# Kernel optimization log

Measured on AMD Instinct MI355X. Metric: run time of the kernel, lower is better.

Reference implementation:

```python
import jax, jax.numpy as jnp
import numpy as np

B, N, E = 16, 2048, 32768   # graphs per batch, nodes per graph, edges per graph
V, D, R, L = 50000, 256, 8, 2  # vocab, embed dim, num relations, gnn layers


def setup_inputs() -> dict:
    key = jax.random.key(0)
    ks = jax.random.split(key, 7)
    nodes = jax.random.randint(ks[0], (B, N), 0, V)
    edges = jax.random.randint(ks[1], (B, 2, E), 0, N)
    types = jax.random.randint(ks[2], (B, E), 0, R)
    emb = jax.random.normal(ks[3], (V, D), jnp.float32) * 0.02
    W = jax.random.normal(ks[4], (L, R, D, D), jnp.float32) * (1.0 / np.sqrt(D))
    W_root = jax.random.normal(ks[5], (L, D, D), jnp.float32) * (1.0 / np.sqrt(D))
    b = jnp.zeros((L, D), jnp.float32)
    return dict(nodes=nodes, edges=edges, types=types, emb=emb, W=W, W_root=W_root, b=b)


def _rgcn_layer(x, src, dst, etype, W, W_root, b):
    # x: [N,D]; src/dst/etype: [E]; W: [R,D,D]; W_root: [D,D]; b: [D]
    n = x.shape[0]
    xw = jnp.einsum('nd,rde->rne', x, W)          # per-relation transform [R,N,D]
    msgs = xw[etype, src]                          # gather per-edge messages [E,D]
    agg = jax.ops.segment_sum(msgs, dst, num_segments=n)          # scatter-add [N,D]
    deg = jax.ops.segment_sum(jnp.ones((src.shape[0],), x.dtype), dst, num_segments=n)
    return agg / jnp.maximum(deg, 1.0)[:, None] + x @ W_root + b  # mean aggr + self loop


def reference(nodes, edges, types, emb, W, W_root, b):
    x = emb[nodes]                                  # [B,N,D] per-sample embedding lookup
    src, dst = edges[:, 0], edges[:, 1]
    layer = jax.vmap(_rgcn_layer, in_axes=(0, 0, 0, 0, None, None, None))
    for l in range(L):
        x = layer(x, src, dst, types, W[l], W_root[l], b[l])
        if l < L - 1:
            x = jax.nn.relu(x)  # dropout is identity at inference
    return x
```

## Files before the change

kernel.cpp:

```cpp
#include <hip/hip_runtime.h>

#define BB 16
#define NN 2048
#define EE 32768
#define DD 256
#define RR 8
#define LL 2
#define BUCKETS (RR * NN)
#define TM 64

typedef unsigned short u16;
typedef __attribute__((__ext_vector_type__(8))) __bf16 bfx8;
typedef __attribute__((__ext_vector_type__(16))) float fx16;

__device__ __forceinline__ float blo(unsigned u){ union{unsigned x;float f;}c; c.x=u<<16; return c.f; }
__device__ __forceinline__ float bhi(unsigned u){ union{unsigned x;float f;}c; c.x=u&0xffff0000u; return c.f; }
__device__ __forceinline__ u16 f2bf(float f){ union{float f;unsigned u;}x; x.f=f;
    return (u16)((x.u + 0x7FFFu + ((x.u>>16)&1u))>>16); }
__device__ __forceinline__ unsigned pk2(float a, float b){
    return (unsigned)f2bf(a) | ((unsigned)f2bf(b)<<16); }

__global__ __launch_bounds__(256) void gather_k(const int* __restrict__ nodes,
                                                const float* __restrict__ emb,
                                                u16* __restrict__ x0,
                                                int b0, int bc)
{
    int t = blockIdx.x * 256 + threadIdx.x;
    int lane = t & 63;
    int row = t >> 6;
    if (row >= bc * NN) return;
    int bb = row / NN;
    int n  = row - bb * NN;
    int v  = nodes[(size_t)(b0 + bb) * NN + n];
    float4 val = *((const float4*)(emb + (size_t)v * DD) + lane);
    ushort4 o;
    o.x = f2bf(val.x); o.y = f2bf(val.y); o.z = f2bf(val.z); o.w = f2bf(val.w);
    *((ushort4*)(x0 + (size_t)row * DD) + lane) = o;
}

__global__ __launch_bounds__(256) void wt_k(const float* __restrict__ W,
                                            const float* __restrict__ Wroot,
                                            u16* __restrict__ Wf)
{
    __shared__ float tl[32][257];
    int ls = blockIdx.y;
    int l = ls / 9, seg = ls - l * 9;
    int kt = blockIdx.x;
    const float* src = (seg < 8) ? W + (size_t)(l * RR + seg) * DD * DD
                                 : Wroot + (size_t)l * DD * DD;
    int t = threadIdx.x;
    for (int k8 = 0; k8 < 32; ++k8)
        tl[k8][t] = src[(size_t)(kt * 32 + k8) * DD + t];
    __syncthreads();
    #pragma unroll
    for (int i = 0; i < 4; ++i) {
        int o = i * 256 + t;
        int fl = o & 63, ks2 = (o >> 6) & 1, nt8 = o >> 7;
        int n = nt8 * 32 + (fl & 31);
        int kb = ks2 * 16 + (fl >> 5) * 8;
        unsigned d0 = pk2(tl[kb + 0][n], tl[kb + 1][n]);
        unsigned d1 = pk2(tl[kb + 2][n], tl[kb + 3][n]);
        unsigned d2 = pk2(tl[kb + 4][n], tl[kb + 5][n]);
        unsigned d3 = pk2(tl[kb + 6][n], tl[kb + 7][n]);
        *(uint4*)(Wf + (((size_t)ls * 8 + kt) * 1024 + o) * 8) =
            make_uint4(d0, d1, d2, d3);
    }
}

__global__ __launch_bounds__(256) void count_k(const int* __restrict__ edges,
                                               const int* __restrict__ types,
                                               int* __restrict__ counts,
                                               int b0, int bc)
{
    int t = blockIdx.x * 256 + threadIdx.x;
    if (t >= bc * EE) return;
    int bb = t / EE;
    int e  = t - bb * EE;
    const int* eb = edges + (size_t)(b0 + bb) * 2 * EE;
    int dst = eb[EE + e];
    int r   = types[(size_t)(b0 + bb) * EE + e];
    atomicAdd(&counts[((size_t)bb * RR + r) * NN + dst], 1);
}

__global__ __launch_bounds__(256) void sect_k(const int* __restrict__ counts,
                                              int* __restrict__ secsum)
{
    __shared__ int red[256];
    int sec = blockIdx.x;
    int t = threadIdx.x;
    size_t base = (size_t)sec * NN;
    int s = 0;
    #pragma unroll
    for (int i = 0; i < 8; ++i) s += counts[base + t * 8 + i];
    red[t] = s;
    __syncthreads();
    for (int off = 128; off > 0; off >>= 1) {
        if (t < off) red[t] += red[t + off];
        __syncthreads();
    }
    if (t == 0) secsum[sec] = red[0];
}

__global__ __launch_bounds__(128) void base_k(const int* __restrict__ secsum,
                                              int* __restrict__ secbase, int nsec)
{
    int t = threadIdx.x;
    if (t >= nsec) return;
    int bb = t >> 3;
    int s = 0;
    for (int i = bb * 8; i < t; ++i) s += secsum[i];
    secbase[t] = s;
}

__global__ __launch_bounds__(256) void offs_k(const int* __restrict__ counts,
                                              const int* __restrict__ secbase,
                                              int* __restrict__ offsets,
                                              int* __restrict__ cursor)
{
    __shared__ int sums[256];
    int sec = blockIdx.x;
    int t = threadIdx.x;
    size_t base = (size_t)sec * NN;
    int v[8], s = 0;
    #pragma unroll
    for (int i = 0; i < 8; ++i) { v[i] = counts[base + t * 8 + i]; s += v[i]; }
    sums[t] = s;
    __syncthreads();
    for (int off = 1; off < 256; off <<= 1) {
        int x = (t >= off) ? sums[t - off] : 0;
        __syncthreads();
        sums[t] += x;
        __syncthreads();
    }
    int run = secbase[sec] + sums[t] - s;
    #pragma unroll
    for (int i = 0; i < 8; ++i) {
        offsets[base + t * 8 + i] = run;
        cursor[base + t * 8 + i]  = run;
        run += v[i];
    }
}

__global__ __launch_bounds__(256) void deg_from_counts(const int* __restrict__ counts,
                                                       float* __restrict__ deg,
                                                       int bc)
{
    int t = blockIdx.x * 256 + threadIdx.x;
    if (t >= bc * NN) return;
    int bb = t / NN;
    int n  = t - bb * NN;
    int d = 0;
    #pragma unroll
    for (int r = 0; r < RR; ++r)
        d += counts[((size_t)bb * RR + r) * NN + n];
    deg[t] = (float)d;
}

__global__ __launch_bounds__(256) void permute_k(const int* __restrict__ edges,
                                                 const int* __restrict__ types,
                                                 int* __restrict__ cursor,
                                                 int* __restrict__ edgeSrc,
                                                 int b0, int bc)
{
    int t = blockIdx.x * 256 + threadIdx.x;
    if (t >= bc * EE) return;
    int bb = t / EE;
    int e  = t - bb * EE;
    const int* eb = edges + (size_t)(b0 + bb) * 2 * EE;
    int src = eb[e];
    int dst = eb[EE + e];
    int r   = types[(size_t)(b0 + bb) * EE + e];
    int pos = atomicAdd(&cursor[((size_t)bb * RR + r) * NN + dst], 1);
    edgeSrc[(size_t)bb * EE + pos] = src;
}

template <int WRITE_BF16>
__global__ __launch_bounds__(512, 4) void rgcn_fused(
    const int* __restrict__ offsets, const int* __restrict__ counts,
    const int* __restrict__ edgeSrc, const u16* __restrict__ xin,
    const u16* __restrict__ Wf,
    const float* __restrict__ bias, const float* __restrict__ deg,
    float* __restrict__ outF, u16* __restrict__ outH, int relu)
{
    __shared__ __align__(16) u16 Af[2 * 16 * 64 * 8];
    __shared__ float sInv[TM];

    int t = threadIdx.x;
    int fl = t & 63;
    int wid = t >> 6;
    int bb = blockIdx.y;
    int m0 = blockIdx.x * TM;

    if (t < TM) sInv[t] = 1.0f / fmaxf(deg[(size_t)bb * NN + m0 + t], 1.0f);

    const u16* xb = xin + (size_t)bb * NN * DD;
    const int* es = edgeSrc + (size_t)bb * EE;

    int gid = t >> 4;
    int j16 = t & 15;
    int ks0 = j16 >> 1;
    int lh2 = j16 & 1;

    fx16 acc[2];
    #pragma unroll
    for (int mt = 0; mt < 2; ++mt)
        #pragma unroll
        for (int e = 0; e < 16; ++e) acc[mt][e] = 0.0f;

    int lh = fl >> 5;

    for (int seg = 0; seg < 9; ++seg) {
        __syncthreads();
        #pragma unroll
        for (int rr = 0; rr < 2; ++rr) {
            int row = gid * 2 + rr;
            int mt = row >> 5, m31 = row & 31;
            int flw = m31 + 32 * lh2;
            unsigned w0, w1, w2, w3, w4, w5, w6, w7;
            if (seg < 8) {
                float a[16];
                #pragma unroll
                for (int e = 0; e < 16; ++e) a[e] = 0.0f;
                int g = ((bb * RR + seg) * NN) + m0 + row;
                int start = offsets[g];
                int cnt   = counts[g];
                for (int jj = 0; jj < cnt; ++jj) {
                    int src = es[start + jj];
                    const u16* xr = xb + (size_t)src * DD;
                    uint4 p0 = *(const uint4*)(xr + j16 * 8);
                    uint4 p1 = *(const uint4*)(xr + 128 + j16 * 8);
                    a[0] += blo(p0.x); a[1] += bhi(p0.x);
                    a[2] += blo(p0.y); a[3] += bhi(p0.y);
                    a[4] += blo(p0.z); a[5] += bhi(p0.z);
                    a[6] += blo(p0.w); a[7] += bhi(p0.w);
                    a[8]  += blo(p1.x); a[9]  += bhi(p1.x);
                    a[10] += blo(p1.y); a[11] += bhi(p1.y);
                    a[12] += blo(p1.z); a[13] += bhi(p1.z);
                    a[14] += blo(p1.w); a[15] += bhi(p1.w);
                }
                w0 = pk2(a[0], a[1]);   w1 = pk2(a[2], a[3]);
                w2 = pk2(a[4], a[5]);   w3 = pk2(a[6], a[7]);
                w4 = pk2(a[8], a[9]);   w5 = pk2(a[10], a[11]);
                w6 = pk2(a[12], a[13]); w7 = pk2(a[14], a[15]);
            } else {
                const u16* xr = xb + (size_t)(m0 + row) * DD;
                uint4 p0 = *(const uint4*)(xr + j16 * 8);
                uint4 p1 = *(const uint4*)(xr + 128 + j16 * 8);
                w0 = p0.x; w1 = p0.y; w2 = p0.z; w3 = p0.w;
                w4 = p1.x; w5 = p1.y; w6 = p1.z; w7 = p1.w;
            }
            int c0 = ((mt * 16 + ks0) * 64 + ((flw + ks0) & 63)) * 8;
            int c1 = ((mt * 16 + ks0 + 8) * 64 + ((flw + ks0 + 8) & 63)) * 8;
            *(uint4*)&Af[c0] = make_uint4(w0, w1, w2, w3);
            *(uint4*)&Af[c1] = make_uint4(w4, w5, w6, w7);
        }
        __syncthreads();

        if (seg == 8) {
            #pragma unroll
            for (int mt = 0; mt < 2; ++mt)
                #pragma unroll
                for (int r = 0; r < 16; ++r) {
                    int rl = mt * 32 + (r & 3) + 8 * (r >> 2) + 4 * lh;
                    acc[mt][r] *= sInv[rl];
                }
        }

        const u16* Wseg = Wf + (size_t)seg * 65536;
        #pragma unroll 2
        for (int kt = 0; kt < 8; ++kt) {
            bfx8 bfr[2], af[2][2];
            #pragma unroll
            for (int ks2 = 0; ks2 < 2; ++ks2) {
                int ksA = kt * 2 + ks2;
                bfr[ks2] = *(const bfx8*)(Wseg + (size_t)kt * 8192 + wid * 1024
                                          + ks2 * 512 + fl * 8);
                af[0][ks2] = *(const bfx8*)&Af[((0  + ksA) * 64 + ((fl + ksA) & 63)) * 8];
                af[1][ks2] = *(const bfx8*)&Af[((16 + ksA) * 64 + ((fl + ksA) & 63)) * 8];
            }
            #pragma unroll
            for (int ks2 = 0; ks2 < 2; ++ks2) {
                acc[0] = __builtin_amdgcn_mfma_f32_32x32x16_bf16(af[0][ks2], bfr[ks2], acc[0], 0, 0, 0);
                acc[1] = __builtin_amdgcn_mfma_f32_32x32x16_bf16(af[1][ks2], bfr[ks2], acc[1], 0, 0, 0);
            }
        }
    }

    int col = wid * 32 + (fl & 31);
    float bv = bias[col];
    #pragma unroll
    for (int mt = 0; mt < 2; ++mt)
        #pragma unroll
        for (int r = 0; r < 16; ++r) {
            int row = m0 + mt * 32 + (r & 3) + 8 * (r >> 2) + 4 * lh;
            float v = acc[mt][r] + bv;
            if (relu) v = fmaxf(v, 0.0f);
            if (WRITE_BF16)
                outH[((size_t)bb * NN + row) * DD + col] = f2bf(v);
            else
                outF[((size_t)bb * NN + row) * DD + col] = v;
        }
}

extern "C" void kernel_launch(void* const* d_in, const int* in_sizes, int n_in,
                              void* d_out, int out_size, void* d_ws, size_t ws_size,
                              hipStream_t stream)
{
    const int*   nodes = (const int*)d_in[0];
    const int*   edges = (const int*)d_in[1];
    const int*   types = (const int*)d_in[2];
    const float* emb   = (const float*)d_in[3];
    const float* W     = (const float*)d_in[4];
    const float* Wroot = (const float*)d_in[5];
    const float* bias  = (const float*)d_in[6];
    float* out = (float*)d_out;

    const size_t wfElems = (size_t)LL * 9 * 8 * 1024 * 8;
    const size_t fixedBytes = wfElems * sizeof(u16) + 256 * sizeof(int);
    const size_t perBatchBytes =
        2 * (size_t)NN * DD * sizeof(u16) + (size_t)NN * sizeof(float) +
        (3 * (size_t)BUCKETS + EE) * sizeof(int);
    int BC = (int)((ws_size - fixedBytes) / perBatchBytes);
    if (BC > BB) BC = BB;
    if (BC < 1) BC = 1;

    u16* Wf      = (u16*)d_ws;
    int* secsum  = (int*)(Wf + wfElems);
    int* secbase = secsum + 128;
    u16* x0      = (u16*)(secbase + 128);
    u16* x1      = x0 + (size_t)BC * NN * DD;
    float* deg   = (float*)(x1 + (size_t)BC * NN * DD);
    int* counts  = (int*)(deg + (size_t)BC * NN);
    int* offsets = counts + (size_t)BC * BUCKETS;
    int* cursor  = offsets + (size_t)BC * BUCKETS;
    int* edgeSrc = cursor + (size_t)BC * BUCKETS;

    wt_k<<<dim3(8, LL * 9), 256, 0, stream>>>(W, Wroot, Wf);

    for (int b0 = 0; b0 < BB; b0 += BC) {
        int bc = BB - b0 < BC ? BB - b0 : BC;

        hipMemsetAsync(counts, 0, (size_t)bc * BUCKETS * sizeof(int), stream);
        gather_k<<<bc * 512, 256, 0, stream>>>(nodes, emb, x0, b0, bc);
        count_k<<<bc * (EE / 256), 256, 0, stream>>>(edges, types, counts, b0, bc);
        sect_k<<<bc * 8, 256, 0, stream>>>(counts, secsum);
        base_k<<<1, 128, 0, stream>>>(secsum, secbase, bc * 8);
        offs_k<<<bc * 8, 256, 0, stream>>>(counts, secbase, offsets, cursor);
        deg_from_counts<<<bc * (NN / 256), 256, 0, stream>>>(counts, deg, bc);
        permute_k<<<bc * (EE / 256), 256, 0, stream>>>(edges, types, cursor, edgeSrc, b0, bc);

        for (int l = 0; l < LL; ++l) {
            const u16* xin = (l == 0) ? x0 : x1;
            const u16* Wfl = Wf + (size_t)l * 9 * 65536;
            dim3 grid(NN / TM, bc);
            if (l == 0)
                rgcn_fused<1><<<grid, 512, 0, stream>>>(offsets, counts, edgeSrc,
                    xin, Wfl, bias + (size_t)l * DD, deg, nullptr, x1, 1);
            else
                rgcn_fused<0><<<grid, 512, 0, stream>>>(offsets, counts, edgeSrc,
                    xin, Wfl, bias + (size_t)l * DD, deg,
                    out + (size_t)b0 * NN * DD, nullptr, 0);
        }
    }
}
```

Baseline: 364.9 us.

## Merge prep kernels, double-buffer gathered A tiles, remap blocks across batches

Merges the preprocessing launches: weight transform with counts zeroing, embedding gather with edge counting, and a single per-batch scan that also computes inverse degree. This cuts launch count and removes the two-level section scan. In the fused layer kernel, the neighbour gather for the next relation segment now goes into a second LDS buffer while the MFMAs for the current segment run. The gather loop is unrolled by two, offsets and counts are staged in shared memory, and block indices are swizzled so neighbouring blocks work on different graphs. The cost is doubled LDS use, which may lower occupancy, and a single-block-per-batch scan that is very serial; the weight transform also now runs once per batch chunk.

```diff
diff --git a/kernel.cpp b/kernel.cpp
--- a/kernel.cpp
+++ b/kernel.cpp
@@ -19,141 +19,116 @@
     return (u16)((x.u + 0x7FFFu + ((x.u>>16)&1u))>>16); }
 __device__ __forceinline__ unsigned pk2(float a, float b){
     return (unsigned)f2bf(a) | ((unsigned)f2bf(b)<<16); }
-
-__global__ __launch_bounds__(256) void gather_k(const int* __restrict__ nodes,
-                                                const float* __restrict__ emb,
-                                                u16* __restrict__ x0,
-                                                int b0, int bc)
-{
-    int t = blockIdx.x * 256 + threadIdx.x;
-    int lane = t & 63;
-    int row = t >> 6;
-    if (row >= bc * NN) return;
-    int bb = row / NN;
-    int n  = row - bb * NN;
-    int v  = nodes[(size_t)(b0 + bb) * NN + n];
-    float4 val = *((const float4*)(emb + (size_t)v * DD) + lane);
-    ushort4 o;
-    o.x = f2bf(val.x); o.y = f2bf(val.y); o.z = f2bf(val.z); o.w = f2bf(val.w);
-    *((ushort4*)(x0 + (size_t)row * DD) + lane) = o;
-}
-
-__global__ __launch_bounds__(256) void wt_k(const float* __restrict__ W,
-                                            const float* __restrict__ Wroot,
-                                            u16* __restrict__ Wf)
-{
-    __shared__ float tl[32][257];
-    int ls = blockIdx.y;
-    int l = ls / 9, seg = ls - l * 9;
-    int kt = blockIdx.x;
-    const float* src = (seg < 8) ? W + (size_t)(l * RR + seg) * DD * DD
-                                 : Wroot + (size_t)l * DD * DD;
+__device__ __forceinline__ void acc8(float* a, uint4 p0, uint4 p1) {
+    a[0]+=blo(p0.x); a[1]+=bhi(p0.x); a[2]+=blo(p0.y); a[3]+=bhi(p0.y);
+    a[4]+=blo(p0.z); a[5]+=bhi(p0.z); a[6]+=blo(p0.w); a[7]+=bhi(p0.w);
+    a[8]+=blo(p1.x); a[9]+=bhi(p1.x); a[10]+=blo(p1.y); a[11]+=bhi(p1.y);
+    a[12]+=blo(p1.z); a[13]+=bhi(p1.z); a[14]+=blo(p1.w); a[15]+=bhi(p1.w);
+}
+
+__global__ __launch_bounds__(256) void prep0(const float* __restrict__ W,
+                                             const float* __restrict__ Wroot,
+                                             u16* __restrict__ Wf,
+                                             int* __restrict__ counts, int bc)
+{
     int t = threadIdx.x;
-    for (int k8 = 0; k8 < 32; ++k8)
-        tl[k8][t] = src[(size_t)(kt * 32 + k8) * DD + t];
-    __syncthreads();
-    #pragma unroll
-    for (int i = 0; i < 4; ++i) {
-        int o = i * 256 + t;
-        int fl = o & 63, ks2 = (o >> 6) & 1, nt8 = o >> 7;
-        int n = nt8 * 32 + (fl & 31);
-        int kb = ks2 * 16 + (fl >> 5) * 8;
-        unsigned d0 = pk2(tl[kb + 0][n], tl[kb + 1][n]);
-        unsigned d1 = pk2(tl[kb + 2][n], tl[kb + 3][n]);
-        unsigned d2 = pk2(tl[kb + 4][n], tl[kb + 5][n]);
-        unsigned d3 = pk2(tl[kb + 6][n], tl[kb + 7][n]);
-        *(uint4*)(Wf + (((size_t)ls * 8 + kt) * 1024 + o) * 8) =
-            make_uint4(d0, d1, d2, d3);
-    }
-}
-
-__global__ __launch_bounds__(256) void count_k(const int* __restrict__ edges,
-                                               const int* __restrict__ types,
-                                               int* __restrict__ counts,
-                                               int b0, int bc)
-{
-    int t = blockIdx.x * 256 + threadIdx.x;
-    if (t >= bc * EE) return;
-    int bb = t / EE;
-    int e  = t - bb * EE;
-    const int* eb = edges + (size_t)(b0 + bb) * 2 * EE;
-    int dst = eb[EE + e];
-    int r   = types[(size_t)(b0 + bb) * EE + e];
-    atomicAdd(&counts[((size_t)bb * RR + r) * NN + dst], 1);
-}
-
-__global__ __launch_bounds__(256) void sect_k(const int* __restrict__ counts,
-                                              int* __restrict__ secsum)
-{
-    __shared__ int red[256];
-    int sec = blockIdx.x;
-    int t = threadIdx.x;
-    size_t base = (size_t)sec * NN;
-    int s = 0;
-    #pragma unroll
-    for (int i = 0; i < 8; ++i) s += counts[base + t * 8 + i];
-    red[t] = s;
-    __syncthreads();
-    for (int off = 128; off > 0; off >>= 1) {
-        if (t < off) red[t] += red[t + off];
+    if (blockIdx.x < 8 * LL * 9) {
+        __shared__ float tl[32][257];
+        int kt = blockIdx.x & 7, ls = blockIdx.x >> 3;
+        int l = ls / 9, seg = ls - l * 9;
+        const float* src = (seg < 8) ? W + (size_t)(l * RR + seg) * DD * DD
+                                     : Wroot + (size_t)l * DD * DD;
+        for (int k8 = 0; k8 < 32; ++k8)
+            tl[k8][t] = src[(size_t)(kt * 32 + k8) * DD + t];
         __syncthreads();
-    }
-    if (t == 0) secsum[sec] = red[0];
-}
-
-__global__ __launch_bounds__(128) void base_k(const int* __restrict__ secsum,
-                                              int* __restrict__ secbase, int nsec)
-{
-    int t = threadIdx.x;
-    if (t >= nsec) return;
-    int bb = t >> 3;
-    int s = 0;
-    for (int i = bb * 8; i < t; ++i) s += secsum[i];
-    secbase[t] = s;
-}
-
-__global__ __launch_bounds__(256) void offs_k(const int* __restrict__ counts,
-                                              const int* __restrict__ secbase,
-                                              int* __restrict__ offsets,
-                                              int* __restrict__ cursor)
-{
+        #pragma unroll
+        for (int i = 0; i < 4; ++i) {
+            int o = i * 256 + t;
+            int fl = o & 63, ks2 = (o >> 6) & 1, nt8 = o >> 7;
+            int n = nt8 * 32 + (fl & 31);
+            int kb = ks2 * 16 + (fl >> 5) * 8;
+            unsigned d0 = pk2(tl[kb + 0][n], tl[kb + 1][n]);
+            unsigned d1 = pk2(tl[kb + 2][n], tl[kb + 3][n]);
+            unsigned d2 = pk2(tl[kb + 4][n], tl[kb + 5][n]);
+            unsigned d3 = pk2(tl[kb + 6][n], tl[kb + 7][n]);
+            *(uint4*)(Wf + (((size_t)ls * 8 + kt) * 1024 + o) * 8) =
+                make_uint4(d0, d1, d2, d3);
+        }
+    } else {
+        int idx = (blockIdx.x - 8 * LL * 9) * 256 + t;
+        int tot = bc * BUCKETS / 4;
+        if (idx < tot) ((int4*)counts)[idx] = make_int4(0, 0, 0, 0);
+    }
+}
+
+__global__ __launch_bounds__(256) void prep1(const int* __restrict__ nodes,
+                                             const float* __restrict__ emb,
+                                             u16* __restrict__ x0,
+                                             const int* __restrict__ edges,
+                                             const int* __restrict__ types,
+                                             int* __restrict__ counts,
+                                             int b0, int bc)
+{
+    int ng = bc * 512;
+    if ((int)blockIdx.x < ng) {
+        int t = blockIdx.x * 256 + threadIdx.x;
+        int lane = t & 63;
+        int row = t >> 6;
+        int bb = row / NN;
+        int n  = row - bb * NN;
+        int v  = nodes[(size_t)(b0 + bb) * NN + n];
+        float4 val = *((const float4*)(emb + (size_t)v * DD) + lane);
+        ushort4 o;
+        o.x = f2bf(val.x); o.y = f2bf(val.y); o.z = f2bf(val.z); o.w = f2bf(val.w);
+        *((ushort4*)(x0 + (size_t)row * DD) + lane) = o;
+    } else {
+        int t = (blockIdx.x - ng) * 256 + threadIdx.x;
+        int bb = t / EE;
+        int e  = t - bb * EE;
+        const int* eb = edges + (size_t)(b0 + bb) * 2 * EE;
+        int dst = eb[EE + e];
+        int r   = types[(size_t)(b0 + bb) * EE + e];
+        atomicAdd(&counts[((size_t)bb * RR + r) * NN + dst], 1);
+    }
+}
+
+__global__ __launch_bounds__(256) void scan2_k(const int* __restrict__ counts,
+                                               int* __restrict__ offsets,
+                                               int* __restrict__ cursor,
+                                               float* __restrict__ invdeg)
+{
+    int bb = blockIdx.x;
+    int tid = threadIdx.x;
+    size_t base = (size_t)bb * BUCKETS;
     __shared__ int sums[256];
-    int sec = blockIdx.x;
-    int t = threadIdx.x;
-    size_t base = (size_t)sec * NN;
-    int v[8], s = 0;
-    #pragma unroll
-    for (int i = 0; i < 8; ++i) { v[i] = counts[base + t * 8 + i]; s += v[i]; }
-    sums[t] = s;
+
+    int tot = 0;
+    #pragma unroll 4
+    for (int i = 0; i < 64; ++i) tot += counts[base + tid * 64 + i];
+    sums[tid] = tot;
     __syncthreads();
     for (int off = 1; off < 256; off <<= 1) {
-        int x = (t >= off) ? sums[t - off] : 0;
+        int v = (tid >= off) ? sums[tid - off] : 0;
         __syncthreads();
-        sums[t] += x;
+        sums[tid] += v;
         __syncthreads();
     }
-    int run = secbase[sec] + sums[t] - s;
+    int run = sums[tid] - tot;
+    for (int i = 0; i < 64; ++i) {
+        size_t idx = base + tid * 64 + i;
+        offsets[idx] = run;
+        cursor[idx]  = run;
+        run += counts[idx];
+    }
     #pragma unroll
     for (int i = 0; i < 8; ++i) {
-        offsets[base + t * 8 + i] = run;
-        cursor[base + t * 8 + i]  = run;
-        run += v[i];
-    }
-}
-
-__global__ __launch_bounds__(256) void deg_from_counts(const int* __restrict__ counts,
-                                                       float* __restrict__ deg,
-                                                       int bc)
-{
-    int t = blockIdx.x * 256 + threadIdx.x;
-    if (t >= bc * NN) return;
-    int bb = t / NN;
-    int n  = t - bb * NN;
-    int d = 0;
-    #pragma unroll
-    for (int r = 0; r < RR; ++r)
-        d += counts[((size_t)bb * RR + r) * NN + n];
-    deg[t] = (float)d;
+        int n = tid * 8 + i;
+        int d = 0;
+        #pragma unroll
+        for (int r = 0; r < RR; ++r)
+            d += counts[base + (size_t)r * NN + n];
+        invdeg[(size_t)bb * NN + n] = 1.0f / fmaxf((float)d, 1.0f);
+    }
 }
 
 __global__ __launch_bounds__(256) void permute_k(const int* __restrict__ edges,
@@ -163,7 +138,6 @@
                                                  int b0, int bc)
 {
     int t = blockIdx.x * 256 + threadIdx.x;
-    if (t >= bc * EE) return;
     int bb = t / EE;
     int e  = t - bb * EE;
     const int* eb = edges + (size_t)(b0 + bb) * 2 * EE;
@@ -174,24 +148,93 @@
     edgeSrc[(size_t)bb * EE + pos] = src;
 }
 
+__device__ __forceinline__ void build_seg(int seg, u16* A,
+                                          const int* sStart, const int* sCnt,
+                                          const int* es, const u16* xb, int m0,
+                                          int gid, int j16, int ks0, int lh2)
+{
+    #pragma unroll
+    for (int rr = 0; rr < 2; ++rr) {
+        int row = gid * 2 + rr;
+        int mt = row >> 5, m31 = row & 31;
+        int flw = m31 + 32 * lh2;
+        unsigned w0, w1, w2, w3, w4, w5, w6, w7;
+        if (seg < 8) {
+            float a[16];
+            #pragma unroll
+            for (int e = 0; e < 16; ++e) a[e] = 0.0f;
+            int start = sStart[seg * TM + row];
+            int cnt   = sCnt[seg * TM + row];
+            const int* ep = es + start;
+            int jj = 0;
+            for (; jj + 2 <= cnt; jj += 2) {
+                int s0 = ep[jj], s1 = ep[jj + 1];
+                const u16* xr0 = xb + (size_t)s0 * DD;
+                const u16* xr1 = xb + (size_t)s1 * DD;
+                uint4 p0 = *(const uint4*)(xr0 + j16 * 8);
+                uint4 p1 = *(const uint4*)(xr0 + 128 + j16 * 8);
+                uint4 q0 = *(const uint4*)(xr1 + j16 * 8);
+                uint4 q1 = *(const uint4*)(xr1 + 128 + j16 * 8);
+                acc8(a, p0, p1);
+                acc8(a, q0, q1);
+            }
+            if (jj < cnt) {
+                const u16* xr0 = xb + (size_t)ep[jj] * DD;
+                uint4 p0 = *(const uint4*)(xr0 + j16 * 8);
+                uint4 p1 = *(const uint4*)(xr0 + 128 + j16 * 8);
+                acc8(a, p0, p1);
+            }
+            w0 = pk2(a[0], a[1]);   w1 = pk2(a[2], a[3]);
+            w2 = pk2(a[4], a[5]);   w3 = pk2(a[6], a[7]);
+            w4 = pk2(a[8], a[9]);   w5 = pk2(a[10], a[11]);
+            w6 = pk2(a[12], a[13]); w7 = pk2(a[14], a[15]);
+        } else {
+            const u16* xr = xb + (size_t)(m0 + row) * DD;
+            uint4 p0 = *(const uint4*)(xr + j16 * 8);
+            uint4 p1 = *(const uint4*)(xr + 128 + j16 * 8);
+            w0 = p0.x; w1 = p0.y; w2 = p0.z; w3 = p0.w;
+            w4 = p1.x; w5 = p1.y; w6 = p1.z; w7 = p1.w;
+        }
+        int c0 = ((mt * 16 + ks0) * 64 + ((flw + ks0) & 63)) * 8;
+        int c1 = ((mt * 16 + ks0 + 8) * 64 + ((flw + ks0 + 8) & 63)) * 8;
+        *(uint4*)&A[c0] = make_uint4(w0, w1, w2, w3);
+        *(uint4*)&A[c1] = make_uint4(w4, w5, w6, w7);
+    }
+}
+
 template <int WRITE_BF16>
 __global__ __launch_bounds__(512, 4) void rgcn_fused(
     const int* __restrict__ offsets, const int* __restrict__ counts,
     const int* __restrict__ edgeSrc, const u16* __restrict__ xin,
     const u16* __restrict__ Wf,
-    const float* __restrict__ bias, const float* __restrict__ deg,
-    float* __restrict__ outF, u16* __restrict__ outH, int relu)
-{
-    __shared__ __align__(16) u16 Af[2 * 16 * 64 * 8];
+    const float* __restrict__ bias, const float* __restrict__ invdeg,
+    float* __restrict__ outF, u16* __restrict__ outH, int relu, int bc)
+{
+    __shared__ __align__(16) u16 Af[2][16384];
     __shared__ float sInv[TM];
+    __shared__ int sStart[8 * TM], sCnt[8 * TM];
 
     int t = threadIdx.x;
     int fl = t & 63;
     int wid = t >> 6;
-    int bb = blockIdx.y;
-    int m0 = blockIdx.x * TM;
-
-    if (t < TM) sInv[t] = 1.0f / fmaxf(deg[(size_t)bb * NN + m0 + t], 1.0f);
+    int bid = blockIdx.x;
+    int bb, mt0;
+    if (bc == 16) {
+        bb  = (bid & 7) * 2 + ((bid >> 3) & 1);
+        mt0 = bid >> 4;
+    } else {
+        bb  = bid >> 5;
+        mt0 = bid & 31;
+    }
+    int m0 = mt0 * TM;
+
+    {
+        int r = t >> 6, row = t & 63;
+        int g = ((bb * RR + r) * NN) + m0 + row;
+        sStart[t] = offsets[g];
+        sCnt[t]   = counts[g];
+    }
+    if (t < TM) sInv[t] = invdeg[(size_t)bb * NN + m0 + t];
 
     const u16* xb = xin + (size_t)bb * NN * DD;
     const int* es = edgeSrc + (size_t)bb * EE;
@@ -200,6 +243,7 @@
     int j16 = t & 15;
     int ks0 = j16 >> 1;
     int lh2 = j16 & 1;
+    int lh = fl >> 5;
 
     fx16 acc[2];
     #pragma unroll
@@ -207,54 +251,14 @@
         #pragma unroll
         for (int e = 0; e < 16; ++e) acc[mt][e] = 0.0f;
 
-    int lh = fl >> 5;
+    __syncthreads();
+    build_seg(0, Af[0], sStart, sCnt, es, xb, m0, gid, j16, ks0, lh2);
+    __syncthreads();
 
     for (int seg = 0; seg < 9; ++seg) {
-        __syncthreads();
-        #pragma unroll
-        for (int rr = 0; rr < 2; ++rr) {
-            int row = gid * 2 + rr;
-            int mt = row >> 5, m31 = row & 31;
-            int flw = m31 + 32 * lh2;
-            unsigned w0, w1, w2, w3, w4, w5, w6, w7;
-            if (seg < 8) {
-                float a[16];
-                #pragma unroll
-                for (int e = 0; e < 16; ++e) a[e] = 0.0f;
-                int g = ((bb * RR + seg) * NN) + m0 + row;
-                int start = offsets[g];
-                int cnt   = counts[g];
-                for (int jj = 0; jj < cnt; ++jj) {
-                    int src = es[start + jj];
-                    const u16* xr = xb + (size_t)src * DD;
-                    uint4 p0 = *(const uint4*)(xr + j16 * 8);
-                    uint4 p1 = *(const uint4*)(xr + 128 + j16 * 8);
-                    a[0] += blo(p0.x); a[1] += bhi(p0.x);
-                    a[2] += blo(p0.y); a[3] += bhi(p0.y);
-                    a[4] += blo(p0.z); a[5] += bhi(p0.z);
-                    a[6] += blo(p0.w); a[7] += bhi(p0.w);
-                    a[8]  += blo(p1.x); a[9]  += bhi(p1.x);
-                    a[10] += blo(p1.y); a[11] += bhi(p1.y);
-                    a[12] += blo(p1.z); a[13] += bhi(p1.z);
-                    a[14] += blo(p1.w); a[15] += bhi(p1.w);
-                }
-                w0 = pk2(a[0], a[1]);   w1 = pk2(a[2], a[3]);
-                w2 = pk2(a[4], a[5]);   w3 = pk2(a[6], a[7]);
-                w4 = pk2(a[8], a[9]);   w5 = pk2(a[10], a[11]);
-                w6 = pk2(a[12], a[13]); w7 = pk2(a[14], a[15]);
-            } else {
-                const u16* xr = xb + (size_t)(m0 + row) * DD;
-                uint4 p0 = *(const uint4*)(xr + j16 * 8);
-                uint4 p1 = *(const uint4*)(xr + 128 + j16 * 8);
-                w0 = p0.x; w1 = p0.y; w2 = p0.z; w3 = p0.w;
-                w4 = p1.x; w5 = p1.y; w6 = p1.z; w7 = p1.w;
-            }
-            int c0 = ((mt * 16 + ks0) * 64 + ((flw + ks0) & 63)) * 8;
-            int c1 = ((mt * 16 + ks0 + 8) * 64 + ((flw + ks0 + 8) & 63)) * 8;
-            *(uint4*)&Af[c0] = make_uint4(w0, w1, w2, w3);
-            *(uint4*)&Af[c1] = make_uint4(w4, w5, w6, w7);
-        }
-        __syncthreads();
+        if (seg < 8)
+            build_seg(seg + 1, Af[(seg + 1) & 1], sStart, sCnt, es, xb, m0,
+                      gid, j16, ks0, lh2);
 
         if (seg == 8) {
             #pragma unroll
@@ -267,6 +271,7 @@
         }
 
         const u16* Wseg = Wf + (size_t)seg * 65536;
+        const u16* A = Af[seg & 1];
         #pragma unroll 2
         for (int kt = 0; kt < 8; ++kt) {
             bfx8 bfr[2], af[2][2];
@@ -275,8 +280,8 @@
                 int ksA = kt * 2 + ks2;
                 bfr[ks2] = *(const bfx8*)(Wseg + (size_t)kt * 8192 + wid * 1024
                                           + ks2 * 512 + fl * 8);
-                af[0][ks2] = *(const bfx8*)&Af[((0  + ksA) * 64 + ((fl + ksA) & 63)) * 8];
-                af[1][ks2] = *(const bfx8*)&Af[((16 + ksA) * 64 + ((fl + ksA) & 63)) * 8];
+                af[0][ks2] = *(const bfx8*)&A[((0  + ksA) * 64 + ((fl + ksA) & 63)) * 8];
+                af[1][ks2] = *(const bfx8*)&A[((16 + ksA) * 64 + ((fl + ksA) & 63)) * 8];
             }
             #pragma unroll
             for (int ks2 = 0; ks2 < 2; ++ks2) {
@@ -284,6 +289,7 @@
                 acc[1] = __builtin_amdgcn_mfma_f32_32x32x16_bf16(af[1][ks2], bfr[ks2], acc[1], 0, 0, 0);
             }
         }
+        __syncthreads();
     }
 
     int col = wid * 32 + (fl & 31);
@@ -316,7 +322,7 @@
     float* out = (float*)d_out;
 
     const size_t wfElems = (size_t)LL * 9 * 8 * 1024 * 8;
-    const size_t fixedBytes = wfElems * sizeof(u16) + 256 * sizeof(int);
+    const size_t fixedBytes = wfElems * sizeof(u16);
     const size_t perBatchBytes =
         2 * (size_t)NN * DD * sizeof(u16) + (size_t)NN * sizeof(float) +
         (3 * (size_t)BUCKETS + EE) * sizeof(int);
@@ -325,41 +331,33 @@
     if (BC < 1) BC = 1;
 
     u16* Wf      = (u16*)d_ws;
-    int* secsum  = (int*)(Wf + wfElems);
-    int* secbase = secsum + 128;
-    u16* x0      = (u16*)(secbase + 128);
+    u16* x0      = Wf + wfElems;
     u16* x1      = x0 + (size_t)BC * NN * DD;
-    float* deg   = (float*)(x1 + (size_t)BC * NN * DD);
-    int* counts  = (int*)(deg + (size_t)BC * NN);
+    float* invdeg = (float*)(x1 + (size_t)BC * NN * DD);
+    int* counts  = (int*)(invdeg + (size_t)BC * NN);
     int* offsets = counts + (size_t)BC * BUCKETS;
     int* cursor  = offsets + (size_t)BC * BUCKETS;
     int* edgeSrc = cursor + (size_t)BC * BUCKETS;
 
-    wt_k<<<dim3(8, LL * 9), 256, 0, stream>>>(W, Wroot, Wf);
-
     for (int b0 = 0; b0 < BB; b0 += BC) {
         int bc = BB - b0 < BC ? BB - b0 : BC;
 
-        hipMemsetAsync(counts, 0, (size_t)bc * BUCKETS * sizeof(int), stream);
-        gather_k<<<bc * 512, 256, 0, stream>>>(nodes, emb, x0, b0, bc);
-        count_k<<<bc * (EE / 256), 256, 0, stream>>>(edges, types, counts, b0, bc);
-        sect_k<<<bc * 8, 256, 0, stream>>>(counts, secsum);
-        base_k<<<1, 128, 0, stream>>>(secsum, secbase, bc * 8);
-        offs_k<<<bc * 8, 256, 0, stream>>>(counts, secbase, offsets, cursor);
-        deg_from_counts<<<bc * (NN / 256), 256, 0, stream>>>(counts, deg, bc);
-        permute_k<<<bc * (EE / 256), 256, 0, stream>>>(edges, types, cursor, edgeSrc, b0, bc);
+        int zeroBlocks = (bc * BUCKETS / 4 + 255) / 256;
+        prep0<<<8 * LL * 9 + zeroBlocks, 256, 0, stream>>>(W, Wroot, Wf, counts, bc);
+        prep1<<<bc * 640, 256, 0, stream>>>(nodes, emb, x0, edges, types, counts, b0, bc);
+        scan2_k<<<bc, 256, 0, stream>>>(counts, offsets, cursor, invdeg);
+        permute_k<<<bc * 128, 256, 0, stream>>>(edges, types, cursor, edgeSrc, b0, bc);
 
         for (int l = 0; l < LL; ++l) {
             const u16* xin = (l == 0) ? x0 : x1;
             const u16* Wfl = Wf + (size_t)l * 9 * 65536;
-            dim3 grid(NN / TM, bc);
             if (l == 0)
-                rgcn_fused<1><<<grid, 512, 0, stream>>>(offsets, counts, edgeSrc,
-                    xin, Wfl, bias + (size_t)l * DD, deg, nullptr, x1, 1);
+                rgcn_fused<1><<<bc * 32, 512, 0, stream>>>(offsets, counts, edgeSrc,
+                    xin, Wfl, bias + (size_t)l * DD, invdeg, nullptr, x1, 1, bc);
             else
-                rgcn_fused<0><<<grid, 512, 0, stream>>>(offsets, counts, edgeSrc,
-                    xin, Wfl, bias + (size_t)l * DD, deg,
-                    out + (size_t)b0 * NN * DD, nullptr, 0);
-        }
-    }
-}
+                rgcn_fused<0><<<bc * 32, 512, 0, stream>>>(offsets, counts, edgeSrc,
+                    xin, Wfl, bias + (size_t)l * DD, invdeg,
+                    out + (size_t)b0 * NN * DD, nullptr, 0, bc);
+        }
+    }
+}
```

After: 301.0 us. 1.21x faster.
